# Performance work log

Measured on AMD Instinct MI355X. Metric: run time of the kernel, lower is better.

Reference implementation:

```python
import jax, jax.numpy as jnp
import numpy as np

INF = 1.0e9
# 8-connected neighborhood (Warcraft shortest-path convention)
DIRS = [(-1, -1), (-1, 0), (-1, 1), (0, -1), (0, 1), (1, -1), (1, 0), (1, 1)]


def _shifted(d_KGG, di, dj):
    # shifted[i, j] = d[i + di, j + dj], INF out of bounds (di, dj static ints)
    K, G, _ = d_KGG.shape
    p = jnp.pad(d_KGG, ((0, 0), (1, 1), (1, 1)), constant_values=INF)
    return p[:, 1 + di:1 + di + G, 1 + dj:1 + dj + G]


def compute_shortest_path(cost_KGG):
    """Vertex-cost shortest path from (0,0) to (G-1,G-1) on an 8-connected grid.
    Returns a 0/1 mask of cells on the optimal path. Bellman-Ford style DP:
    G*G relaxation sweeps guarantee convergence for positive costs."""
    K, G, _ = cost_KGG.shape
    dist0 = jnp.full((K, G, G), INF, dtype=cost_KGG.dtype).at[:, 0, 0].set(cost_KGG[:, 0, 0])

    def relax(_, dist):
        nbr = dist  # placeholder; fold min over 8 shifted copies
        nbr = _shifted(dist, *DIRS[0])
        for d in DIRS[1:]:
            nbr = jnp.minimum(nbr, _shifted(dist, *d))
        return jnp.minimum(dist, cost_KGG + nbr)

    dist = jax.lax.fori_loop(0, G * G, relax, dist0)

    # Backtrack from (G-1, G-1): predecessor = argmin dist over 8 neighbors.
    di = jnp.array([d[0] for d in DIRS])
    dj = jnp.array([d[1] for d in DIRS])
    ks = jnp.arange(K)

    def step(carry, _):
        mask, pi, pj = carry
        ci = pi[:, None] + di[None, :]   # [K, 8]
        cj = pj[:, None] + dj[None, :]
        valid = (ci >= 0) & (ci < G) & (cj >= 0) & (cj < G)
        cic = jnp.clip(ci, 0, G - 1)
        cjc = jnp.clip(cj, 0, G - 1)
        nd = jnp.where(valid, dist[ks[:, None], cic, cjc], INF)
        best = jnp.argmin(nd, axis=-1)  # [K]
        npi = jnp.take_along_axis(cic, best[:, None], 1)[:, 0]
        npj = jnp.take_along_axis(cjc, best[:, None], 1)[:, 0]
        done = (pi == 0) & (pj == 0)
        pi2 = jnp.where(done, pi, npi)
        pj2 = jnp.where(done, pj, npj)
        mask2 = mask.at[ks, pi2, pj2].set(1.0)
        return (mask2, pi2, pj2), None

    mask0 = jnp.zeros((K, G, G), jnp.float32).at[:, G - 1, G - 1].set(1.0)
    p0 = jnp.full((K,), G - 1, dtype=jnp.int32)
    (mask, _, _), _ = jax.lax.scan(step, (mask0, p0, p0), None, length=G * G)
    return mask


def setup_inputs() -> dict:
    key = jax.random.key(0)
    S, B, G, n_costs = 8, 1024, 12, 5
    w_SBW = jax.random.randint(jax.random.fold_in(key, 1), (S, B, G * G), 0, n_costs)
    costs_t = jnp.array([0.8, 1.2, 5.3, 7.7, 9.2], dtype=jnp.float32)
    return {"w_SBW": w_SBW, "costs_t": costs_t}


def reference(w_SBW, costs_t):
    S, B, W = w_SBW.shape
    G = int(np.sqrt(W))
    w_KGG = w_SBW.reshape(S * B, G, G)
    cost_KGG = costs_t[w_KGG]          # embedding-style gather of per-cell costs
    y_KGG = compute_shortest_path(cost_KGG)
    return y_KGG.reshape(S, B, W).astype(jnp.int32)  # .long() in the original
```

## Files before the change

### kernel.cpp

```cpp
#include <hip/hip_runtime.h>
#include <float.h>

#define GDIM 12
#define NC   144
#define FINF 1.0e9f

template<int CTRL>
__device__ inline float rot(float x) {
    return __int_as_float(__builtin_amdgcn_update_dpp(
        __float_as_int(x), __float_as_int(x), CTRL, 0xf, 0xf, false));
}

#define ROWU(i, C, D) {                                                    \
    float V = ((i) == 0)        ? D[1] :                                   \
              ((i) == GDIM - 1) ? D[GDIM - 2] :                            \
              fminf(D[(i) > 0 ? (i)-1 : 0], D[(i) < GDIM-1 ? (i)+1 : GDIM-1]); \
    float cm3 = fminf(V, D[(i)]);                                          \
    float nbr = fminf(fminf(rot<0x121>(cm3), rot<0x12F>(cm3)), V);         \
    D[(i)] = fminf(D[(i)], C[(i)] + nbr); }

#define SWEEP_DN(C, D) { _Pragma("unroll")                                 \
    for (int i = 0; i < GDIM; ++i) ROWU(i, C, D) }
#define SWEEP_UP(C, D) { _Pragma("unroll")                                 \
    for (int q = 0; q < GDIM; ++q) { const int i = GDIM - 1 - q; ROWU(i, C, D) } }

__global__ __launch_bounds__(512)
void path_kernel(const int* __restrict__ w,
                 const float* __restrict__ costs,
                 int* __restrict__ out) {
    const int t  = threadIdx.x;
    const int wv = t >> 6;
    const int l  = t & 63;
    const int g  = l >> 4;
    const int j  = l & 15;
    const int pw = blockIdx.x * 32 + wv * 4;

    __shared__ int4  s_w4[8][NC];
    __shared__ float dl[8][4][200];
    __shared__ int   ml[8][4 * NC];

    const int4* wvp = (const int4*)(w + (size_t)pw * NC);
    int4 wA = wvp[l];
    int4 wB = wvp[64 + l];
    int4 wC = (l < 16) ? wvp[128 + l] : make_int4(0, 0, 0, 0);

    const float cv0 = costs[0], cv1 = costs[1], cv2 = costs[2],
                cv3 = costs[3], cv4 = costs[4];

    int* mlw = ml[wv];
    #pragma unroll
    for (int q = 0; q < 9; ++q) mlw[q * 64 + l] = 0;
    float* dlw = &dl[wv][0][0];
    #pragma unroll
    for (int q = 0; q < 13; ++q) { int idx = q * 64 + l; if (idx < 800) dlw[idx] = FINF; }

    s_w4[wv][l] = wA;
    s_w4[wv][64 + l] = wB;
    if (l < 16) s_w4[wv][128 + l] = wC;

    const bool act = (j < GDIM);
    const int* sw = (const int*)s_w4[wv];
    float* A = &dl[wv][g][0];

    float c[GDIM], ct[GDIM], d[GDIM];
    #pragma unroll
    for (int i = 0; i < GDIM; ++i) {
        int wiN = sw[g * NC + i * GDIM + (act ? j : 0)];
        int wiT = sw[act ? (g * NC + j * GDIM + i) : 0];
        float cN = cv4, cT = cv4;
        cN = (wiN == 0) ? cv0 : cN;  cT = (wiT == 0) ? cv0 : cT;
        cN = (wiN == 1) ? cv1 : cN;  cT = (wiT == 1) ? cv1 : cT;
        cN = (wiN == 2) ? cv2 : cN;  cT = (wiT == 2) ? cv2 : cT;
        cN = (wiN == 3) ? cv3 : cN;  cT = (wiT == 3) ? cv3 : cT;
        c[i]  = act ? cN : FINF;
        ct[i] = act ? cT : FINF;
        d[i]  = FINF;
    }
    if (j == 0) d[0] = c[0];

    #pragma unroll 1
    for (int cyc = 0; cyc < 40; ++cyc) {
        float dp[GDIM];
        #pragma unroll
        for (int i = 0; i < GDIM; ++i) dp[i] = d[i];

        SWEEP_DN(c, d)
        SWEEP_UP(c, d)

        if (act) {
            #pragma unroll
            for (int i = 0; i < GDIM; ++i) A[(i + 1) * 14 + (j + 1)] = d[i];
            #pragma unroll
            for (int i = 0; i < GDIM; ++i) d[i] = A[(j + 1) * 14 + (i + 1)];
        }

        SWEEP_DN(ct, d)
        SWEEP_UP(ct, d)

        if (act) {
            #pragma unroll
            for (int i = 0; i < GDIM; ++i) A[(j + 1) * 14 + (i + 1)] = d[i];
            #pragma unroll
            for (int i = 0; i < GDIM; ++i) d[i] = A[(i + 1) * 14 + (j + 1)];
        }

        bool ch = false;
        #pragma unroll
        for (int i = 0; i < GDIM; ++i) ch = ch | (d[i] < dp[i]);
        if (__ballot(ch) == 0ull) break;
    }

    {
        int* mlg = mlw + g * NC;
        const int offj = (j < 3) ? (j - 15) : (j == 3) ? -1 : (j == 4) ? 1 : (j + 8);
        int a = 12 * 14 + 12;
        int n = NC - 1;
        if (j == 0) mlg[n] = 1;
        const int target = 1 * 14 + 1;
        for (int s = 0; s < NC; ++s) {
            if (__ballot(a != target) == 0ull) break;
            float v = (j < 8) ? A[a + offj] : FINF;
            float m = v;
            m = fminf(m, rot<0xB1>(m));
            m = fminf(m, rot<0x4E>(m));
            m = fminf(m, rot<0x141>(m));
            m = fminf(m, rot<0x140>(m));
            unsigned long long bal = __ballot((j < 8) & (v == m));
            int mask8 = (int)(bal >> (g * 16)) & 0xFF;
            int bidx = __ffs(mask8) - 1;
            if (a != target) {
                int off = (bidx < 3) ? (bidx - 15) : (bidx == 3) ? -1
                        : (bidx == 4) ? 1 : (bidx + 8);
                int adj = (bidx < 3) ? 2 : (bidx > 4) ? -2 : 0;
                a += off;
                n += off + adj;
                if (j == 0) mlg[n] = 1;
            }
        }
    }

    int4* ov = (int4*)(out + (size_t)pw * NC);
    const int4* ml4w = (const int4*)mlw;
    ov[l] = ml4w[l];
    ov[64 + l] = ml4w[64 + l];
    if (l < 16) ov[128 + l] = ml4w[128 + l];
}

extern "C" void kernel_launch(void* const* d_in, const int* in_sizes, int n_in,
                              void* d_out, int out_size, void* d_ws, size_t ws_size,
                              hipStream_t stream) {
    const int*   w     = (const int*)d_in[0];
    const float* costs = (const float*)d_in[1];
    int*         out   = (int*)d_out;
    const int K = in_sizes[0] / NC;
    path_kernel<<<dim3(K / 32), dim3(512), 0, stream>>>(w, costs, out);
}
```

Before: 20.94 us.

## Write path mask directly to global, interleave row sweeps, skip early convergence checks

Drops the shared-memory mask buffer. The output is now zeroed in global memory at kernel start and the backtrack scatters path cells straight to global, which removes the LDS round trip and the final copy. The row-update order inside each sweep is interleaved (0,6,1,7,...), likely to expose independent work to the scheduler, although each update still reads its neighbour rows. The convergence ballot and the snapshot copy are skipped for the first two cycles. It relies on the global zero stores completing before the scattered ones, via an explicit vmcnt wait, and the reordered sweep may change convergence speed per cycle.

```diff
diff --git a/kernel.cpp b/kernel.cpp
--- a/kernel.cpp
+++ b/kernel.cpp
@@ -19,10 +19,14 @@
     float nbr = fminf(fminf(rot<0x121>(cm3), rot<0x12F>(cm3)), V);         \
     D[(i)] = fminf(D[(i)], C[(i)] + nbr); }
 
-#define SWEEP_DN(C, D) { _Pragma("unroll")                                 \
-    for (int i = 0; i < GDIM; ++i) ROWU(i, C, D) }
-#define SWEEP_UP(C, D) { _Pragma("unroll")                                 \
-    for (int q = 0; q < GDIM; ++q) { const int i = GDIM - 1 - q; ROWU(i, C, D) } }
+#define SWEEP_DN2(C, D) {                                                  \
+    ROWU(0,C,D) ROWU(6,C,D) ROWU(1,C,D) ROWU(7,C,D)                        \
+    ROWU(2,C,D) ROWU(8,C,D) ROWU(3,C,D) ROWU(9,C,D)                        \
+    ROWU(4,C,D) ROWU(10,C,D) ROWU(5,C,D) ROWU(11,C,D) }
+#define SWEEP_UP2(C, D) {                                                  \
+    ROWU(11,C,D) ROWU(5,C,D) ROWU(10,C,D) ROWU(4,C,D)                      \
+    ROWU(9,C,D) ROWU(3,C,D) ROWU(8,C,D) ROWU(2,C,D)                        \
+    ROWU(7,C,D) ROWU(1,C,D) ROWU(6,C,D) ROWU(0,C,D) }
 
 __global__ __launch_bounds__(512)
 void path_kernel(const int* __restrict__ w,
@@ -37,19 +41,23 @@
 
     __shared__ int4  s_w4[8][NC];
     __shared__ float dl[8][4][200];
-    __shared__ int   ml[8][4 * NC];
 
     const int4* wvp = (const int4*)(w + (size_t)pw * NC);
     int4 wA = wvp[l];
     int4 wB = wvp[64 + l];
     int4 wC = (l < 16) ? wvp[128 + l] : make_int4(0, 0, 0, 0);
 
+    {
+        int4* ov = (int4*)(out + (size_t)pw * NC);
+        const int4 z = make_int4(0, 0, 0, 0);
+        ov[l] = z;
+        ov[64 + l] = z;
+        if (l < 16) ov[128 + l] = z;
+    }
+
     const float cv0 = costs[0], cv1 = costs[1], cv2 = costs[2],
                 cv3 = costs[3], cv4 = costs[4];
 
-    int* mlw = ml[wv];
-    #pragma unroll
-    for (int q = 0; q < 9; ++q) mlw[q * 64 + l] = 0;
     float* dlw = &dl[wv][0][0];
     #pragma unroll
     for (int q = 0; q < 13; ++q) { int idx = q * 64 + l; if (idx < 800) dlw[idx] = FINF; }
@@ -80,12 +88,15 @@
 
     #pragma unroll 1
     for (int cyc = 0; cyc < 40; ++cyc) {
+        const bool chk = (cyc >= 2);
         float dp[GDIM];
-        #pragma unroll
-        for (int i = 0; i < GDIM; ++i) dp[i] = d[i];
+        if (chk) {
+            #pragma unroll
+            for (int i = 0; i < GDIM; ++i) dp[i] = d[i];
+        }
 
-        SWEEP_DN(c, d)
-        SWEEP_UP(c, d)
+        SWEEP_DN2(c, d)
+        SWEEP_UP2(c, d)
 
         if (act) {
             #pragma unroll
@@ -94,8 +105,8 @@
             for (int i = 0; i < GDIM; ++i) d[i] = A[(j + 1) * 14 + (i + 1)];
         }
 
-        SWEEP_DN(ct, d)
-        SWEEP_UP(ct, d)
+        SWEEP_DN2(ct, d)
+        SWEEP_UP2(ct, d)
 
         if (act) {
             #pragma unroll
@@ -104,18 +115,22 @@
             for (int i = 0; i < GDIM; ++i) d[i] = A[(i + 1) * 14 + (j + 1)];
         }
 
-        bool ch = false;
-        #pragma unroll
-        for (int i = 0; i < GDIM; ++i) ch = ch | (d[i] < dp[i]);
-        if (__ballot(ch) == 0ull) break;
+        if (chk) {
+            bool ch = false;
+            #pragma unroll
+            for (int i = 0; i < GDIM; ++i) ch = ch | (d[i] < dp[i]);
+            if (__ballot(ch) == 0ull) break;
+        }
     }
 
+    asm volatile("s_waitcnt vmcnt(0)" ::: "memory");
+
     {
-        int* mlg = mlw + g * NC;
+        int* outg = out + (size_t)(pw + g) * NC;
         const int offj = (j < 3) ? (j - 15) : (j == 3) ? -1 : (j == 4) ? 1 : (j + 8);
         int a = 12 * 14 + 12;
         int n = NC - 1;
-        if (j == 0) mlg[n] = 1;
+        if (j == 0) outg[n] = 1;
         const int target = 1 * 14 + 1;
         for (int s = 0; s < NC; ++s) {
             if (__ballot(a != target) == 0ull) break;
@@ -134,16 +149,10 @@
                 int adj = (bidx < 3) ? 2 : (bidx > 4) ? -2 : 0;
                 a += off;
                 n += off + adj;
-                if (j == 0) mlg[n] = 1;
+                if (j == 0) outg[n] = 1;
             }
         }
     }
-
-    int4* ov = (int4*)(out + (size_t)pw * NC);
-    const int4* ml4w = (const int4*)mlw;
-    ov[l] = ml4w[l];
-    ov[64 + l] = ml4w[64 + l];
-    if (l < 16) ov[128 + l] = ml4w[128 + l];
 }
 
 extern "C" void kernel_launch(void* const* d_in, const int* in_sizes, int n_in,
```

Result: slower. 21.78 us (+4.0%).
